# Optimization experiments

Measured on AMD Instinct MI355X. Metric: run time of the kernel, lower is better.

Reference implementation:

```python
import jax, jax.numpy as jnp
import numpy as np
import math
from jax.scipy.special import erfc

KE = 14.3996
ALPHA = 0.3
CUTOFF = 6.0
KMAX = 12
N, M, PER = 32768, 8, 4096
P = 2097152
F_R_CUT = math.erfc(math.sqrt(ALPHA) * CUTOFF) / CUTOFF
BORN_CUT = 1.0  # placeholder; 1/CUTOFF**n computed per-pair below


def _make_kvecs():
    # torch: krange = [0..kmax, -1..-kmax], cartesian_prod(kr, kr, [0]), filter norm
    kr = np.concatenate([np.arange(0, KMAX + 1), -np.arange(1, KMAX + 1)]).astype(np.float32)
    kx, ky = np.meshgrid(kr, kr, indexing='ij')
    kv = np.stack([kx.ravel(), ky.ravel(), np.zeros(kx.size, np.float32)], axis=1)
    nrm = (kv ** 2).sum(1)
    keep = (nrm <= KMAX ** 2 + 2) & (nrm != 0)
    return jnp.asarray(kv[keep])

KVECS = _make_kvecs()  # [K,3]


def _energy(q, R_shift, cell, offsets, r0_ij, n_ij, idx_i, idx_j, idx_m):
    seg_p = idx_m[idx_i]  # molecule id of each pair
    r_ij = R_shift[idx_j] - R_shift[idx_i] + offsets
    d = jnp.linalg.norm(r_ij, axis=1)
    mask = d < CUTOFF
    d_safe = jnp.where(mask, d, 1.0)
    # real space (erfc-screened, shifted at cutoff)
    f_r = erfc(jnp.sqrt(jnp.asarray(ALPHA, q.dtype)) * d_safe) / d_safe
    pot = q[idx_i] * q[idx_j] * (f_r - F_R_CUT)
    pot = jnp.where(mask, pot, 0.0)
    y_real = 0.5 * KE * jax.ops.segment_sum(pot, seg_p, num_segments=M)
    # Born repulsion
    q_ij = jnp.abs(q[idx_i] * q[idx_j])
    B_ij = q_ij * r0_ij ** (n_ij - 1.0) / n_ij
    born = B_ij * (1.0 / d_safe ** n_ij - 1.0 / CUTOFF ** n_ij)
    born = jnp.where(mask, born, 0.0)
    y_born = 0.5 * KE * jax.ops.segment_sum(born, seg_p, num_segments=M)
    # reciprocal space
    recip = 2.0 * jnp.pi * jnp.swapaxes(jnp.linalg.inv(cell), 1, 2)  # [M,3,3]
    vbox = jnp.abs(jnp.linalg.det(cell))  # [M]
    kv = jnp.einsum('kd,mde->mke', KVECS, recip)  # [M,K,3]
    ksq = jnp.sum(kv ** 2, axis=2)  # [M,K]
    q_gauss = jnp.exp(-0.25 * ksq / ALPHA)
    kdp = jnp.einsum('nke,ne->nk', kv[idx_m], R_shift)  # [N,K]
    q_real = jax.ops.segment_sum(q[:, None] * jnp.cos(kdp), idx_m, num_segments=M)
    q_imag = jax.ops.segment_sum(q[:, None] * jnp.sin(kdp), idx_m, num_segments=M)
    q_dens = q_real ** 2 + q_imag ** 2
    y_ew = (2.0 * jnp.pi / vbox) * jnp.sum(q_dens * q_gauss / ksq, axis=1)
    self_int = jnp.sqrt(jnp.asarray(ALPHA / np.pi, q.dtype)) * jax.ops.segment_sum(q ** 2, idx_m, num_segments=M)
    y_slab = KE * (2.0 * jnp.pi / vbox) * jnp.sum(q * R_shift[:, 2]) ** 2
    y_recip = KE * (y_ew - self_int) + y_slab
    y_coulomb = y_real + y_recip
    return y_coulomb + y_born, y_coulomb, y_born


def setup_inputs() -> dict:
    key = jax.random.key(0)
    ks = jax.random.split(key, 8)
    q = jax.random.normal(ks[0], (N,), dtype=jnp.float32) * 0.5
    R = jax.random.uniform(ks[1], (N, 3), dtype=jnp.float32) * 20.0
    shift = jax.random.normal(ks[2], (M, 3), dtype=jnp.float32) * 0.5
    cell = jnp.tile(jnp.eye(3, dtype=jnp.float32) * 20.0, (M, 1, 1))
    offsets = jnp.zeros((P, 3), dtype=jnp.float32)
    r0_ij = jax.random.uniform(ks[3], (P,), minval=1.5, maxval=3.0, dtype=jnp.float32)
    n_ij = jax.random.uniform(ks[4], (P,), minval=6.0, maxval=12.0, dtype=jnp.float32)
    idx_i = jax.random.randint(ks[5], (P,), 0, N, dtype=jnp.int32)
    step = jax.random.randint(ks[6], (P,), 1, PER, dtype=jnp.int32)
    idx_j = (idx_i // PER) * PER + (idx_i % PER + step) % PER  # same molecule, j != i
    idx_m = jnp.repeat(jnp.arange(M, dtype=jnp.int32), PER)
    is_film = jax.random.randint(ks[7], (N,), 0, 2, dtype=jnp.int32)
    return {'q': q, 'R': R, 'shift': shift, 'cell': cell, 'offsets': offsets,
            'r0_ij': r0_ij, 'n_ij': n_ij, 'idx_i': idx_i, 'idx_j': idx_j,
            'idx_m': idx_m, 'is_film': is_film}


def reference(q, R, shift, cell, offsets, r0_ij, n_ij, idx_i, idx_j, idx_m, is_film):
    film = is_film.astype(q.dtype)[:, None]  # substrate atoms get zero shift/force

    def rshift_of(s):
        return R + s[idx_m] * film

    R_shift = rshift_of(shift)
    y_energy, y_coulomb, y_born = _energy(q, R_shift, cell, offsets, r0_ij, n_ij, idx_i, idx_j, idx_m)

    def film_force_norm_fn(s):
        X = rshift_of(s)
        g = jax.grad(lambda X_: jnp.sum(_energy(q, X_, cell, offsets, r0_ij, n_ij, idx_i, idx_j, idx_m)[0]))(X)
        dEdR = -g * film  # zero substrate forces
        film_force = jax.ops.segment_sum(dEdR, idx_m, num_segments=M)  # [M,3]
        return jnp.sum(film_force ** 2, axis=1)  # ||f||^2 per molecule

    film_force_norm = film_force_norm_fn(shift)
    film_norm_grad = jax.grad(lambda s: jnp.sum(film_force_norm_fn(s)))(shift)
    return y_energy, y_coulomb, y_born, film_force_norm, film_norm_grad
```

## Files before the change

### kernel.cpp

```cpp
#include <hip/hip_runtime.h>
#include <math.h>

#define NATOM 32768
#define NMOL 8
#define PERM 4096
#define LOG2PERM 12
#define NPAIR 2097152
#define NKKH 312
#define CAPREC 262144
#define PPB 2048
#define NFILT (NPAIR/PPB)
#define NSFB (NMOL*50)
#define PB1 256
#define FCAP 512

#define KE_C 14.3996f
#define ALPHA_C 0.3f
#define SQRT_ALPHA_C 0.5477225575051661f
#define ACONST_C 0.6180387232371366f
#define SELF_C 0.3090193616185683f
#define TWO_PI_C 6.283185307179586f
#define LN_CUTOFF_C 1.791759469228055f

typedef float vf4 __attribute__((ext_vector_type(4)));
typedef int   vi4 __attribute__((ext_vector_type(4)));


__device__ float4 g_X[NATOM];
__device__ float4 g_TH[NATOM];
__device__ float4 g_kvch[NMOL*NKKH];
__device__ float2 g_S[NMOL*NKKH];
__device__ float2 g_Sf[NMOL*NKKH];
__device__ float4 g_recA[CAPREC];
__device__ float4 g_recB[CAPREC];
__device__ int   g_nrec;
__device__ float g_recipM[NMOL][9];
__device__ float g_vbox[NMOL];
__device__ float g_self[NMOL], g_qfilm[NMOL];
__device__ float g_yreal[NMOL], g_yborn[NMOL];
__device__ float g_SG[NMOL][3];
__device__ float g_SH[NMOL][3];
__device__ float g_Fm[NMOL][3];
__device__ float g_SHr[NMOL][3];
__device__ float g_D, g_C2, g_FRC;

__device__ __forceinline__ float waveReduce(float v){
#pragma unroll
    for (int off = 32; off > 0; off >>= 1) v += __shfl_down(v, off, 64);
    return v;
}

__device__ __forceinline__ vf4 ntloadf4(const float4* p){
    return __builtin_nontemporal_load((const vf4*)p);
}
__device__ __forceinline__ vi4 ntloadi4(const int* p){
    return __builtin_nontemporal_load((const vi4*)p);
}
__device__ __forceinline__ vf4 ntloadv4(const float* p){
    return __builtin_nontemporal_load((const vf4*)p);
}
__device__ __forceinline__ void ntstoref4(float4* p, float a, float b, float c, float d){
    vf4 v = {a, b, c, d};
    __builtin_nontemporal_store(v, (vf4*)p);
}

__device__ __forceinline__ float frcp(float x){ return __builtin_amdgcn_rcpf(x); }

__device__ __forceinline__ float erfc_fast(float x, float expt){
    float t = frcp(1.f + 0.3275911f*x);
    return expt*t*(0.254829592f + t*(-0.284496736f + t*(1.421413741f +
                   t*(-1.453152027f + t*1.061405429f))));
}

__device__ __forceinline__ void pair_body(float rx, float ry, float rz, float d2v,
                                          float r0, float nij, float qq, int fm,
                                          float* s_acc, float FRC){
    int m = fm & 7;
    float d = sqrtf(d2v);
    float inv_d = frcp(d);
    float logd = 0.5f*__logf(d2v);
    float Bc = fabsf(qq)*__expf((nij - 1.f)*__logf(r0))*frcp(nij);
    float expt = __expf(-ALPHA_C*d2v);
    float er = erfc_fast(SQRT_ALPHA_C*d, expt);
    float dmn = __expf(-nij*logd);
    float fp = -ACONST_C*expt*inv_d - er*inv_d*inv_d;
    float Up = 0.5f*KE_C*(qq*fp - Bc*nij*dmn*inv_d);
    atomicAdd(&s_acc[m*5+3], qq*(er*inv_d - FRC));
    atomicAdd(&s_acc[m*5+4], Bc*(dmn - __expf(-nij*LN_CUTOFF_C)));
    if (fm & 8){
        float fdiff = (fm & 16) ? 1.f : -1.f;
        float sc = Up*inv_d*fdiff;
        atomicAdd(&s_acc[m*5+0], sc*rx);
        atomicAdd(&s_acc[m*5+1], sc*ry);
        atomicAdd(&s_acc[m*5+2], sc*rz);
    }
}

__device__ __forceinline__ void invCell(const float* c, float rm[9], float& vb){
    float a=c[0],b=c[1],cc=c[2],d=c[3],e=c[4],f=c[5],g=c[6],h=c[7],i=c[8];
    float det = a*(e*i - f*h) - b*(d*i - f*g) + cc*(d*h - e*g);
    float inv = 1.f/det;
    rm[0]=TWO_PI_C*(e*i-f*h)*inv;  rm[1]=TWO_PI_C*(f*g-d*i)*inv;  rm[2]=TWO_PI_C*(d*h-e*g)*inv;
    rm[3]=TWO_PI_C*(cc*h-b*i)*inv; rm[4]=TWO_PI_C*(a*i-cc*g)*inv; rm[5]=TWO_PI_C*(b*g-a*h)*inv;
    rm[6]=TWO_PI_C*(b*f-cc*e)*inv; rm[7]=TWO_PI_C*(cc*d-a*f)*inv; rm[8]=TWO_PI_C*(a*e-b*d)*inv;
    vb = fabsf(det);
}

__global__ __launch_bounds__(256) void k_init(const float* cell, const float* q,
                                              const float* R, const float* shift,
                                              const int* is_film){
    __shared__ float s_rm[NMOL][9];
    __shared__ float s_vb[NMOL];
    __shared__ float red[12];
    int tid = threadIdx.x;
    if (tid < NMOL){
        float rm[9], vb;
        invCell(cell + 9*tid, rm, vb);
#pragma unroll
        for (int k = 0; k < 9; ++k) s_rm[tid][k] = rm[k];
        s_vb[tid] = vb;
    }
    __syncthreads();
    if (blockIdx.x == 0){
        if (tid < NMOL){
#pragma unroll
            for (int k = 0; k < 9; ++k) g_recipM[tid][k] = s_rm[tid][k];
            g_vbox[tid] = s_vb[tid];
        }
        if (tid == 0){
            float c2 = 0.f;
            for (int mm = 0; mm < NMOL; ++mm) c2 += TWO_PI_C/s_vb[mm];
            g_C2 = c2;
            g_FRC = (float)(erfc(sqrt(0.3)*6.0)/6.0);
        }
        for (int id = tid; id < NMOL*NKKH; id += 256){
            int m = id / NKKH, h = id % NKKH;
            int kx, ky;
            if (h < 12){ kx = 0; ky = h + 1; }
            else { int t = h - 12; kx = t/25 + 1; ky = t%25 - 12; }
            float fkx = (float)kx, fky = (float)ky;
            float nrm = fkx*fkx + fky*fky;
            float kvx = fkx*s_rm[m][0] + fky*s_rm[m][3];
            float kvy = fkx*s_rm[m][1] + fky*s_rm[m][4];
            float kvz = fkx*s_rm[m][2] + fky*s_rm[m][5];
            float coef = 0.f;
            if (nrm <= 146.f){
                float ksq = kvx*kvx + kvy*kvy + kvz*kvz;
                coef = (TWO_PI_C/s_vb[m]) * expf(-0.25f*ksq/ALPHA_C) / ksq;
            }
            g_kvch[id] = make_float4(kvx, kvy, kvz, coef);
        }
    } else {
        int n = (blockIdx.x - 1)*256 + tid;
        int m = n >> LOG2PERM;
        int film = is_film[n];
        float qn = q[n];
        float x = R[3*n+0], y = R[3*n+1], z = R[3*n+2];
        if (film){ x += shift[3*m+0]; y += shift[3*m+1]; z += shift[3*m+2]; }
        unsigned qb = (__float_as_uint(qn) & ~1u) | (unsigned)film;
        g_X[n] = make_float4(x, y, z, __uint_as_float(qb));
        float qf = film ? qn : 0.f;
        float th1 = s_rm[m][0]*x + s_rm[m][1]*y + s_rm[m][2]*z;
        float th2 = s_rm[m][3]*x + s_rm[m][4]*y + s_rm[m][5]*z;
        g_TH[n] = make_float4(th1, th2, qn, qf);
        float vD = waveReduce(qn*z);
        float vS = waveReduce(qn*qn);
        float vQ = waveReduce(qf);
        int lane = tid & 63, w = tid >> 6;
        if (!lane){ red[w] = vD; red[4+w] = vS; red[8+w] = vQ; }
        __syncthreads();
        if (tid == 0){
            unsafeAtomicAdd(&g_D, red[0]+red[1]+red[2]+red[3]);
            unsafeAtomicAdd(&g_self[m], red[4]+red[5]+red[6]+red[7]);
            unsafeAtomicAdd(&g_qfilm[m], red[8]+red[9]+red[10]+red[11]);
        }
    }
}

__global__ __launch_bounds__(256) void k_fsf(const int* idx_i, const int* idx_j,
                                             const float* r0_ij, const float* n_ij){
    __shared__ float s_rx[FCAP], s_ry[FCAP], s_rz[FCAP], s_d2[FCAP];
    __shared__ float s_r0[FCAP], s_nn[FCAP], s_qq[FCAP];
    __shared__ int   s_fm[FCAP];
    __shared__ float s_acc[NMOL*5];
    __shared__ float s_red[160];
    __shared__ int s_cnt, s_cnt2, s_base, s_wcur;
    int tid = threadIdx.x;
    int lane = tid & 63, wid = tid >> 6;
    if (blockIdx.x < NFILT){
        if (tid < NMOL*5) s_acc[tid] = 0.f;
        if (tid == 0){ s_cnt = 0; s_cnt2 = 0; s_wcur = 0; }
        __syncthreads();
        float FRC = g_FRC;
        int p0 = blockIdx.x*PPB + tid*8;
        vi4 ii0 = ntloadi4(idx_i + p0), ii1 = ntloadi4(idx_i + p0 + 4);
        vi4 jj0 = ntloadi4(idx_j + p0), jj1 = ntloadi4(idx_j + p0 + 4);
        vf4 r0q0 = ntloadv4(r0_ij + p0), r0q1 = ntloadv4(r0_ij + p0 + 4);
        vf4 nq0  = ntloadv4(n_ij + p0),  nq1  = ntloadv4(n_ij + p0 + 4);
        int ia[8] = {ii0.x, ii0.y, ii0.z, ii0.w, ii1.x, ii1.y, ii1.z, ii1.w};
        int ja[8] = {jj0.x, jj0.y, jj0.z, jj0.w, jj1.x, jj1.y, jj1.z, jj1.w};
        float r0a[8] = {r0q0.x, r0q0.y, r0q0.z, r0q0.w, r0q1.x, r0q1.y, r0q1.z, r0q1.w};
        float na[8]  = {nq0.x, nq0.y, nq0.z, nq0.w, nq1.x, nq1.y, nq1.z, nq1.w};
        float4 xi[8], xj[8];
#pragma unroll
        for (int k = 0; k < 8; ++k){ xi[k] = g_X[ia[k]]; xj[k] = g_X[ja[k]]; }
#pragma unroll
        for (int k = 0; k < 8; ++k){
            float rx = xj[k].x - xi[k].x;
            float ry = xj[k].y - xi[k].y;
            float rz = xj[k].z - xi[k].z;
            float d2v = rx*rx + ry*ry + rz*rz;
            if (d2v < 36.f){
                unsigned fi = __float_as_uint(xi[k].w) & 1u;
                unsigned fj = __float_as_uint(xj[k].w) & 1u;
                int fm = (ia[k] >> LOG2PERM) | ((fi != fj) ? 8 : 0) | (fj ? 16 : 0);
                float qq = xi[k].w*xj[k].w;
                int slot = atomicAdd(&s_cnt, 1);
                if (slot < FCAP){
                    if (fi != fj) atomicAdd(&s_cnt2, 1);
                    s_rx[slot]=rx; s_ry[slot]=ry; s_rz[slot]=rz; s_d2[slot]=d2v;
                    s_r0[slot]=r0a[k]; s_nn[slot]=na[k]; s_qq[slot]=qq; s_fm[slot]=fm;
                } else {
                    pair_body(rx, ry, rz, d2v, r0a[k], na[k], qq, fm, s_acc, FRC);
                    if (fi != fj){
                        int gs = atomicAdd(&g_nrec, 1);
                        if (gs < CAPREC){
                            ntstoref4(&g_recA[gs], rx, ry, rz, d2v);
                            ntstoref4(&g_recB[gs], r0a[k], na[k], qq, (float)fm);
                        }
                    }
                }
            }
        }
        __syncthreads();
        int cnt = s_cnt; if (cnt > FCAP) cnt = FCAP;
        if (tid == 0) s_base = atomicAdd(&g_nrec, s_cnt2);
        __syncthreads();
        int base = s_base;
        for (int r = tid; r < cnt; r += 256){
            float rx=s_rx[r], ry=s_ry[r], rz=s_rz[r], d2v=s_d2[r];
            float r0=s_r0[r], nij=s_nn[r], qq=s_qq[r];
            int fm = s_fm[r];
            pair_body(rx, ry, rz, d2v, r0, nij, qq, fm, s_acc, FRC);
            if (fm & 8){
                int gs = base + atomicAdd(&s_wcur, 1);
                if (gs < CAPREC){
                    ntstoref4(&g_recA[gs], rx, ry, rz, d2v);
                    ntstoref4(&g_recB[gs], r0, nij, qq, (float)fm);
                }
            }
        }
        __syncthreads();
        if (tid < NMOL*5){
            float v = s_acc[tid];
            if (v != 0.f){
                int m = tid/5, c = tid%5;
                if (c < 3) unsafeAtomicAdd(&g_SG[m][c], v);
                else if (c == 3) unsafeAtomicAdd(&g_yreal[m], v);
                else unsafeAtomicAdd(&g_yborn[m], v);
            }
        }
    } else {
        int sb = blockIdx.x - NFILT;
        int m = sb / 50, c = sb % 50;
        int kx, ky0, h0, len;
        if (c < 2){ kx = 0; ky0 = 1 + 8*c; h0 = 8*c; len = c ? 4 : 8; }
        else { int t = c - 2; kx = t/4 + 1; int s4 = t%4; ky0 = -12 + 8*s4; h0 = 12 + (kx-1)*25 + 8*s4; len = (s4==3) ? 1 : 8; }
        float fkx = (float)kx, fky0 = (float)ky0;
        int base = m << LOG2PERM;
        float aR[8], aI[8], bR[8], bI[8];
#pragma unroll
        for (int e = 0; e < 8; ++e){ aR[e]=0.f; aI[e]=0.f; bR[e]=0.f; bI[e]=0.f; }
        for (int a = 0; a < 16; ++a){
            float4 th = g_TH[base + tid + a*256];
            float s, cc, s2, c2;
            __sincosf(fkx*th.x + fky0*th.y, &s, &cc);
            __sincosf(th.y, &s2, &c2);
            float qv = th.z, qf = th.w;
#pragma unroll
            for (int e = 0; e < 8; ++e){
                aR[e] += qv*cc; aI[e] += qv*s;
                bR[e] += qf*cc; bI[e] += qf*s;
                float nc = cc*c2 - s*s2;
                float ns = cc*s2 + s*c2;
                cc = nc; s = ns;
            }
        }
#pragma unroll
        for (int e = 0; e < 8; ++e){
            float v0 = waveReduce(aR[e]), v1 = waveReduce(aI[e]);
            float v2 = waveReduce(bR[e]), v3 = waveReduce(bI[e]);
            if (!lane){
                s_red[(e*4+0)*4+wid] = v0; s_red[(e*4+1)*4+wid] = v1;
                s_red[(e*4+2)*4+wid] = v2; s_red[(e*4+3)*4+wid] = v3;
            }
        }
        __syncthreads();
        if (tid < 32){
            float v = s_red[tid*4+0]+s_red[tid*4+1]+s_red[tid*4+2]+s_red[tid*4+3];
            int e = tid >> 2, comp = tid & 3;
            if (e < len){
                int idx = m*NKKH + h0 + e;
                if (comp == 0) g_S[idx].x = v;
                else if (comp == 1) g_S[idx].y = v;
                else if (comp == 2) g_Sf[idx].x = v;
                else g_Sf[idx].y = v;
            }
        }
    }
}

__global__ __launch_bounds__(512) void k_mid(float* out){
    __shared__ float s_F[NMOL][3];
    __shared__ float s_Dd;
    int tid = threadIdx.x;
    int m = tid >> 6, lane = tid & 63;
    float gx = 0.f, gy = 0.f, gz = 0.f, yew = 0.f;
    for (int h = lane; h < NKKH; h += 64){
        float4 kv = g_kvch[m*NKKH + h];
        float2 S = g_S[m*NKKH + h];
        float2 Sf = g_Sf[m*NKKH + h];
        float w = kv.w*(S.y*Sf.x - S.x*Sf.y);
        gx += w*kv.x; gy += w*kv.y; gz += w*kv.z;
        yew += kv.w*(S.x*S.x + S.y*S.y);
    }
    gx = waveReduce(gx); gy = waveReduce(gy); gz = waveReduce(gz); yew = waveReduce(yew);
    if (lane == 0){
        float D = g_D, qfm = g_qfilm[m];
        float sgrx = 4.f*KE_C*gx;
        float sgry = 4.f*KE_C*gy;
        float sgrz = 4.f*KE_C*gz + 2.f*KE_C*g_C2*D*qfm;
        float fx = -(g_SG[m][0] + sgrx);
        float fy = -(g_SG[m][1] + sgry);
        float fz = -(g_SG[m][2] + sgrz);
        s_F[m][0] = fx; s_F[m][1] = fy; s_F[m][2] = fz;
        g_Fm[m][0] = fx; g_Fm[m][1] = fy; g_Fm[m][2] = fz;
        float yslab = KE_C*(TWO_PI_C/g_vbox[m])*D*D;
        float yrecip = KE_C*(2.f*yew - SELF_C*g_self[m]) + yslab;
        float yr = 0.5f*KE_C*g_yreal[m];
        float yb = 0.5f*KE_C*g_yborn[m];
        float yc = yr + yrecip;
        out[0  + m] = yc + yb;
        out[8  + m] = yc;
        out[16 + m] = yb;
        out[24 + m] = fx*fx + fy*fy + fz*fz;
    }
    __syncthreads();
    if (tid == 0){
        float dd = 0.f;
        for (int mm = 0; mm < NMOL; ++mm) dd += s_F[mm][2]*g_qfilm[mm];
        s_Dd = dd;
    }
    __syncthreads();
    float Fx = s_F[m][0], Fy = s_F[m][1], Fz = s_F[m][2];
    float hx = 0.f, hy = 0.f, hz = 0.f;
    for (int h = lane; h < NKKH; h += 64){
        float4 kv = g_kvch[m*NKKH + h];
        float2 S = g_S[m*NKKH + h];
        float2 Sf = g_Sf[m*NKKH + h];
        float kF = kv.x*Fx + kv.y*Fy + kv.z*Fz;
        float w = kv.w*kF*((Sf.x*Sf.x + Sf.y*Sf.y) - (S.x*Sf.x + S.y*Sf.y));
        hx += w*kv.x; hy += w*kv.y; hz += w*kv.z;
    }
    hx = waveReduce(hx); hy = waveReduce(hy); hz = waveReduce(hz);
    if (lane == 0){
        g_SHr[m][0] = 4.f*KE_C*hx;
        g_SHr[m][1] = 4.f*KE_C*hy;
        g_SHr[m][2] = 4.f*KE_C*hz + 2.f*KE_C*g_C2*s_Dd*g_qfilm[m];
    }
}

__global__ __launch_bounds__(256) void k_pass1(){
    __shared__ float s_F[NMOL*3];
    __shared__ float s_hv[NMOL*3];
    int tid = threadIdx.x;
    if (tid < NMOL*3){
        s_F[tid] = g_Fm[tid/3][tid%3];
        s_hv[tid] = 0.f;
    }
    __syncthreads();
    int nrec = g_nrec; if (nrec > CAPREC) nrec = CAPREC;
    for (int r = blockIdx.x*256 + tid; r < nrec; r += PB1*256){
        vf4 A = ntloadf4(&g_recA[r]);
        vf4 B = ntloadf4(&g_recB[r]);
        int fm = (int)B.w;
        int m = fm & 7;
        float rx = A.x, ry = A.y, rz = A.z, d2 = A.w;
        float r0 = B.x, nij = B.y, qq = B.z;
        float Fx = s_F[m*3+0], Fy = s_F[m*3+1], Fz = s_F[m*3+2];
        float d = sqrtf(d2);
        float inv_d = frcp(d);
        float logd = 0.5f*__logf(d2);
        float Bc = fabsf(qq)*__expf((nij - 1.f)*__logf(r0))*frcp(nij);
        float expt = __expf(-ALPHA_C*d2);
        float er = erfc_fast(SQRT_ALPHA_C*d, expt);
        float dmn = __expf(-nij*logd);
        float fp = -ACONST_C*expt*inv_d - er*inv_d*inv_d;
        float Up = 0.5f*KE_C*(qq*fp - Bc*nij*dmn*inv_d);
        float fpp = ACONST_C*expt*(2.f*ALPHA_C + 2.f*inv_d*inv_d) + 2.f*er*inv_d*inv_d*inv_d;
        float Upp = 0.5f*KE_C*(qq*fpp + Bc*nij*(nij+1.f)*dmn*inv_d*inv_d);
        float ui = Up*inv_d;
        float ddot = (rx*Fx + ry*Fy + rz*Fz)*inv_d;
        float c1 = (Upp - ui)*ddot*inv_d;
        atomicAdd(&s_hv[m*3+0], c1*rx + ui*Fx);
        atomicAdd(&s_hv[m*3+1], c1*ry + ui*Fy);
        atomicAdd(&s_hv[m*3+2], c1*rz + ui*Fz);
    }
    __syncthreads();
    if (tid < NMOL*3){
        float v = s_hv[tid];
        if (v != 0.f) unsafeAtomicAdd(&g_SH[tid/3][tid%3], v);
    }
}

__global__ __launch_bounds__(64) void k_final(float* out){
    int tid = threadIdx.x;
    if (tid < NMOL*3){
        int m = tid/3, c = tid%3;
        out[32 + tid] = -2.f*(g_SH[m][c] + g_SHr[m][c]);
    }
    __syncthreads();
    if (tid < NMOL){
        g_self[tid] = 0.f; g_qfilm[tid] = 0.f;
        g_yreal[tid] = 0.f; g_yborn[tid] = 0.f;
#pragma unroll
        for (int c = 0; c < 3; ++c){ g_SG[tid][c] = 0.f; g_SH[tid][c] = 0.f; }
    }
    if (tid == 0){ g_D = 0.f; g_nrec = 0; }
}

extern "C" void kernel_launch(void* const* d_in, const int* in_sizes, int n_in,
                              void* d_out, int out_size, void* d_ws, size_t ws_size,
                              hipStream_t stream){
    const float* q       = (const float*)d_in[0];
    const float* R       = (const float*)d_in[1];
    const float* shift   = (const float*)d_in[2];
    const float* cell    = (const float*)d_in[3];
    const float* r0_ij   = (const float*)d_in[5];
    const float* n_ij    = (const float*)d_in[6];
    const int*   idx_i   = (const int*)d_in[7];
    const int*   idx_j   = (const int*)d_in[8];
    const int*   is_film = (const int*)d_in[10];
    float* out = (float*)d_out;

    k_init<<<dim3(1 + NATOM/256), dim3(256), 0, stream>>>(cell, q, R, shift, is_film);
    k_fsf<<<dim3(NFILT + NSFB), dim3(256), 0, stream>>>(idx_i, idx_j, r0_ij, n_ij);
    k_mid<<<dim3(1), dim3(512), 0, stream>>>(out);
    k_pass1<<<dim3(PB1), dim3(256), 0, stream>>>();
    k_final<<<dim3(1), dim3(64), 0, stream>>>(out);
}
```

Baseline: 61.66 us.

## Fold Hessian-vector pass into per-molecule second-moment tensor accumulated in filter kernel

The Hessian-vector product over cross film/substrate pairs is linear in the per-molecule force vector, so each pair now accumulates a symmetric rr^T weight tensor and a scalar sum in the first pair pass. The mid kernel contracts these with F at the end. This removes the record buffer writes and reads, the k_pass1 and k_final launches, and the global record counter. In exchange, the first pass does extra atomics per cross pair, which is offset somewhat by using per-wave shared accumulators. Precision may differ slightly because of the reordered summation.

```diff
diff --git a/kernel.cpp b/kernel.cpp
--- a/kernel.cpp
+++ b/kernel.cpp
@@ -7,12 +7,11 @@
 #define LOG2PERM 12
 #define NPAIR 2097152
 #define NKKH 312
-#define CAPREC 262144
 #define PPB 2048
 #define NFILT (NPAIR/PPB)
 #define NSFB (NMOL*50)
-#define PB1 256
 #define FCAP 512
+#define NACC 12
 
 #define KE_C 14.3996f
 #define ALPHA_C 0.3f
@@ -31,17 +30,12 @@
 __device__ float4 g_kvch[NMOL*NKKH];
 __device__ float2 g_S[NMOL*NKKH];
 __device__ float2 g_Sf[NMOL*NKKH];
-__device__ float4 g_recA[CAPREC];
-__device__ float4 g_recB[CAPREC];
-__device__ int   g_nrec;
 __device__ float g_recipM[NMOL][9];
 __device__ float g_vbox[NMOL];
 __device__ float g_self[NMOL], g_qfilm[NMOL];
 __device__ float g_yreal[NMOL], g_yborn[NMOL];
 __device__ float g_SG[NMOL][3];
-__device__ float g_SH[NMOL][3];
-__device__ float g_Fm[NMOL][3];
-__device__ float g_SHr[NMOL][3];
+__device__ float g_M[NMOL][7];
 __device__ float g_D, g_C2, g_FRC;
 
 __device__ __forceinline__ float waveReduce(float v){
@@ -50,18 +44,11 @@
     return v;
 }
 
-__device__ __forceinline__ vf4 ntloadf4(const float4* p){
-    return __builtin_nontemporal_load((const vf4*)p);
-}
 __device__ __forceinline__ vi4 ntloadi4(const int* p){
     return __builtin_nontemporal_load((const vi4*)p);
 }
 __device__ __forceinline__ vf4 ntloadv4(const float* p){
     return __builtin_nontemporal_load((const vf4*)p);
-}
-__device__ __forceinline__ void ntstoref4(float4* p, float a, float b, float c, float d){
-    vf4 v = {a, b, c, d};
-    __builtin_nontemporal_store(v, (vf4*)p);
 }
 
 __device__ __forceinline__ float frcp(float x){ return __builtin_amdgcn_rcpf(x); }
@@ -74,8 +61,9 @@
 
 __device__ __forceinline__ void pair_body(float rx, float ry, float rz, float d2v,
                                           float r0, float nij, float qq, int fm,
-                                          float* s_acc, float FRC){
+                                          float* accW, float FRC){
     int m = fm & 7;
+    float* a = accW + m*NACC;
     float d = sqrtf(d2v);
     float inv_d = frcp(d);
     float logd = 0.5f*__logf(d2v);
@@ -85,14 +73,25 @@
     float dmn = __expf(-nij*logd);
     float fp = -ACONST_C*expt*inv_d - er*inv_d*inv_d;
     float Up = 0.5f*KE_C*(qq*fp - Bc*nij*dmn*inv_d);
-    atomicAdd(&s_acc[m*5+3], qq*(er*inv_d - FRC));
-    atomicAdd(&s_acc[m*5+4], Bc*(dmn - __expf(-nij*LN_CUTOFF_C)));
+    atomicAdd(&a[3], qq*(er*inv_d - FRC));
+    atomicAdd(&a[4], Bc*(dmn - __expf(-nij*LN_CUTOFF_C)));
     if (fm & 8){
         float fdiff = (fm & 16) ? 1.f : -1.f;
         float sc = Up*inv_d*fdiff;
-        atomicAdd(&s_acc[m*5+0], sc*rx);
-        atomicAdd(&s_acc[m*5+1], sc*ry);
-        atomicAdd(&s_acc[m*5+2], sc*rz);
+        atomicAdd(&a[0], sc*rx);
+        atomicAdd(&a[1], sc*ry);
+        atomicAdd(&a[2], sc*rz);
+        float ui = Up*inv_d;
+        float fpp = ACONST_C*expt*(2.f*ALPHA_C + 2.f*inv_d*inv_d) + 2.f*er*inv_d*inv_d*inv_d;
+        float Upp = 0.5f*KE_C*(qq*fpp + Bc*nij*(nij+1.f)*dmn*inv_d*inv_d);
+        float w = (Upp - ui)*frcp(d2v);
+        atomicAdd(&a[5],  w*rx*rx);
+        atomicAdd(&a[6],  w*ry*ry);
+        atomicAdd(&a[7],  w*rz*rz);
+        atomicAdd(&a[8],  w*rx*ry);
+        atomicAdd(&a[9],  w*rx*rz);
+        atomicAdd(&a[10], w*ry*rz);
+        atomicAdd(&a[11], ui);
     }
 }
 
@@ -182,15 +181,16 @@
     __shared__ float s_rx[FCAP], s_ry[FCAP], s_rz[FCAP], s_d2[FCAP];
     __shared__ float s_r0[FCAP], s_nn[FCAP], s_qq[FCAP];
     __shared__ int   s_fm[FCAP];
-    __shared__ float s_acc[NMOL*5];
+    __shared__ float s_accW[4*NMOL*NACC];
     __shared__ float s_red[160];
-    __shared__ int s_cnt, s_cnt2, s_base, s_wcur;
+    __shared__ int s_cnt;
     int tid = threadIdx.x;
     int lane = tid & 63, wid = tid >> 6;
     if (blockIdx.x < NFILT){
-        if (tid < NMOL*5) s_acc[tid] = 0.f;
-        if (tid == 0){ s_cnt = 0; s_cnt2 = 0; s_wcur = 0; }
-        __syncthreads();
+        for (int a = tid; a < 4*NMOL*NACC; a += 256) s_accW[a] = 0.f;
+        if (tid == 0) s_cnt = 0;
+        __syncthreads();
+        float* accW = s_accW + wid*(NMOL*NACC);
         float FRC = g_FRC;
         int p0 = blockIdx.x*PPB + tid*8;
         vi4 ii0 = ntloadi4(idx_i + p0), ii1 = ntloadi4(idx_i + p0 + 4);
@@ -217,47 +217,29 @@
                 float qq = xi[k].w*xj[k].w;
                 int slot = atomicAdd(&s_cnt, 1);
                 if (slot < FCAP){
-                    if (fi != fj) atomicAdd(&s_cnt2, 1);
                     s_rx[slot]=rx; s_ry[slot]=ry; s_rz[slot]=rz; s_d2[slot]=d2v;
                     s_r0[slot]=r0a[k]; s_nn[slot]=na[k]; s_qq[slot]=qq; s_fm[slot]=fm;
                 } else {
-                    pair_body(rx, ry, rz, d2v, r0a[k], na[k], qq, fm, s_acc, FRC);
-                    if (fi != fj){
-                        int gs = atomicAdd(&g_nrec, 1);
-                        if (gs < CAPREC){
-                            ntstoref4(&g_recA[gs], rx, ry, rz, d2v);
-                            ntstoref4(&g_recB[gs], r0a[k], na[k], qq, (float)fm);
-                        }
-                    }
+                    pair_body(rx, ry, rz, d2v, r0a[k], na[k], qq, fm, accW, FRC);
                 }
             }
         }
         __syncthreads();
         int cnt = s_cnt; if (cnt > FCAP) cnt = FCAP;
-        if (tid == 0) s_base = atomicAdd(&g_nrec, s_cnt2);
-        __syncthreads();
-        int base = s_base;
         for (int r = tid; r < cnt; r += 256){
-            float rx=s_rx[r], ry=s_ry[r], rz=s_rz[r], d2v=s_d2[r];
-            float r0=s_r0[r], nij=s_nn[r], qq=s_qq[r];
-            int fm = s_fm[r];
-            pair_body(rx, ry, rz, d2v, r0, nij, qq, fm, s_acc, FRC);
-            if (fm & 8){
-                int gs = base + atomicAdd(&s_wcur, 1);
-                if (gs < CAPREC){
-                    ntstoref4(&g_recA[gs], rx, ry, rz, d2v);
-                    ntstoref4(&g_recB[gs], r0, nij, qq, (float)fm);
-                }
-            }
-        }
-        __syncthreads();
-        if (tid < NMOL*5){
-            float v = s_acc[tid];
+            pair_body(s_rx[r], s_ry[r], s_rz[r], s_d2[r],
+                      s_r0[r], s_nn[r], s_qq[r], s_fm[r], accW, FRC);
+        }
+        __syncthreads();
+        if (tid < NMOL*NACC){
+            float v = s_accW[tid] + s_accW[NMOL*NACC + tid]
+                    + s_accW[2*NMOL*NACC + tid] + s_accW[3*NMOL*NACC + tid];
             if (v != 0.f){
-                int m = tid/5, c = tid%5;
+                int m = tid/NACC, c = tid%NACC;
                 if (c < 3) unsafeAtomicAdd(&g_SG[m][c], v);
                 else if (c == 3) unsafeAtomicAdd(&g_yreal[m], v);
-                else unsafeAtomicAdd(&g_yborn[m], v);
+                else if (c == 4) unsafeAtomicAdd(&g_yborn[m], v);
+                else unsafeAtomicAdd(&g_M[m][c-5], v);
             }
         }
     } else {
@@ -334,7 +316,6 @@
         float fy = -(g_SG[m][1] + sgry);
         float fz = -(g_SG[m][2] + sgrz);
         s_F[m][0] = fx; s_F[m][1] = fy; s_F[m][2] = fz;
-        g_Fm[m][0] = fx; g_Fm[m][1] = fy; g_Fm[m][2] = fz;
         float yslab = KE_C*(TWO_PI_C/g_vbox[m])*D*D;
         float yrecip = KE_C*(2.f*yew - SELF_C*g_self[m]) + yslab;
         float yr = 0.5f*KE_C*g_yreal[m];
@@ -364,69 +345,29 @@
     }
     hx = waveReduce(hx); hy = waveReduce(hy); hz = waveReduce(hz);
     if (lane == 0){
-        g_SHr[m][0] = 4.f*KE_C*hx;
-        g_SHr[m][1] = 4.f*KE_C*hy;
-        g_SHr[m][2] = 4.f*KE_C*hz + 2.f*KE_C*g_C2*s_Dd*g_qfilm[m];
-    }
-}
-
-__global__ __launch_bounds__(256) void k_pass1(){
-    __shared__ float s_F[NMOL*3];
-    __shared__ float s_hv[NMOL*3];
-    int tid = threadIdx.x;
-    if (tid < NMOL*3){
-        s_F[tid] = g_Fm[tid/3][tid%3];
-        s_hv[tid] = 0.f;
-    }
-    __syncthreads();
-    int nrec = g_nrec; if (nrec > CAPREC) nrec = CAPREC;
-    for (int r = blockIdx.x*256 + tid; r < nrec; r += PB1*256){
-        vf4 A = ntloadf4(&g_recA[r]);
-        vf4 B = ntloadf4(&g_recB[r]);
-        int fm = (int)B.w;
-        int m = fm & 7;
-        float rx = A.x, ry = A.y, rz = A.z, d2 = A.w;
-        float r0 = B.x, nij = B.y, qq = B.z;
-        float Fx = s_F[m*3+0], Fy = s_F[m*3+1], Fz = s_F[m*3+2];
-        float d = sqrtf(d2);
-        float inv_d = frcp(d);
-        float logd = 0.5f*__logf(d2);
-        float Bc = fabsf(qq)*__expf((nij - 1.f)*__logf(r0))*frcp(nij);
-        float expt = __expf(-ALPHA_C*d2);
-        float er = erfc_fast(SQRT_ALPHA_C*d, expt);
-        float dmn = __expf(-nij*logd);
-        float fp = -ACONST_C*expt*inv_d - er*inv_d*inv_d;
-        float Up = 0.5f*KE_C*(qq*fp - Bc*nij*dmn*inv_d);
-        float fpp = ACONST_C*expt*(2.f*ALPHA_C + 2.f*inv_d*inv_d) + 2.f*er*inv_d*inv_d*inv_d;
-        float Upp = 0.5f*KE_C*(qq*fpp + Bc*nij*(nij+1.f)*dmn*inv_d*inv_d);
-        float ui = Up*inv_d;
-        float ddot = (rx*Fx + ry*Fy + rz*Fz)*inv_d;
-        float c1 = (Upp - ui)*ddot*inv_d;
-        atomicAdd(&s_hv[m*3+0], c1*rx + ui*Fx);
-        atomicAdd(&s_hv[m*3+1], c1*ry + ui*Fy);
-        atomicAdd(&s_hv[m*3+2], c1*rz + ui*Fz);
-    }
-    __syncthreads();
-    if (tid < NMOL*3){
-        float v = s_hv[tid];
-        if (v != 0.f) unsafeAtomicAdd(&g_SH[tid/3][tid%3], v);
-    }
-}
-
-__global__ __launch_bounds__(64) void k_final(float* out){
-    int tid = threadIdx.x;
-    if (tid < NMOL*3){
-        int m = tid/3, c = tid%3;
-        out[32 + tid] = -2.f*(g_SH[m][c] + g_SHr[m][c]);
+        float shrx = 4.f*KE_C*hx;
+        float shry = 4.f*KE_C*hy;
+        float shrz = 4.f*KE_C*hz + 2.f*KE_C*g_C2*s_Dd*g_qfilm[m];
+        float Pxx = g_M[m][0], Pyy = g_M[m][1], Pzz = g_M[m][2];
+        float Pxy = g_M[m][3], Pxz = g_M[m][4], Pyz = g_M[m][5];
+        float sU  = g_M[m][6];
+        float shpx = Pxx*Fx + Pxy*Fy + Pxz*Fz + sU*Fx;
+        float shpy = Pxy*Fx + Pyy*Fy + Pyz*Fz + sU*Fy;
+        float shpz = Pxz*Fx + Pyz*Fy + Pzz*Fz + sU*Fz;
+        out[32 + 3*m + 0] = -2.f*(shpx + shrx);
+        out[32 + 3*m + 1] = -2.f*(shpy + shry);
+        out[32 + 3*m + 2] = -2.f*(shpz + shrz);
     }
     __syncthreads();
     if (tid < NMOL){
         g_self[tid] = 0.f; g_qfilm[tid] = 0.f;
         g_yreal[tid] = 0.f; g_yborn[tid] = 0.f;
 #pragma unroll
-        for (int c = 0; c < 3; ++c){ g_SG[tid][c] = 0.f; g_SH[tid][c] = 0.f; }
-    }
-    if (tid == 0){ g_D = 0.f; g_nrec = 0; }
+        for (int c = 0; c < 3; ++c) g_SG[tid][c] = 0.f;
+#pragma unroll
+        for (int c = 0; c < 7; ++c) g_M[tid][c] = 0.f;
+    }
+    if (tid == 0) g_D = 0.f;
 }
 
 extern "C" void kernel_launch(void* const* d_in, const int* in_sizes, int n_in,
@@ -446,6 +387,4 @@
     k_init<<<dim3(1 + NATOM/256), dim3(256), 0, stream>>>(cell, q, R, shift, is_film);
     k_fsf<<<dim3(NFILT + NSFB), dim3(256), 0, stream>>>(idx_i, idx_j, r0_ij, n_ij);
     k_mid<<<dim3(1), dim3(512), 0, stream>>>(out);
-    k_pass1<<<dim3(PB1), dim3(256), 0, stream>>>();
-    k_final<<<dim3(1), dim3(64), 0, stream>>>(out);
-}
+}
```

After: 79.37 us. 28.7% more time.
